# Kernel tuning notes

Hardware: AMD Instinct MI355X
Metric: run time of the kernel (lower is better)

The kernel has to match this reference:

```python
import jax, jax.numpy as jnp
import numpy as np
from jax import lax

L_MAX = 3          # n_ang_mom: l = 0, 1, 2
M_DIM = 2 * L_MAX - 1  # magnetic components, padded to 5
N_PAIRS = 40000
N_FEAT = 128


def hermite_features(g, n_features):
    """Orthonormal Hermite-function features h_0..h_{F-1}(g); [n] -> [n, F].

    Stable recurrence: h_{k+1} = sqrt(2/(k+1)) g h_k - sqrt(k/(k+1)) h_{k-1}.
    """
    h0 = (np.pi ** -0.25) * jnp.exp(-0.5 * g * g)
    h1 = jnp.sqrt(jnp.asarray(2.0, g.dtype)) * g * h0

    def step(carry, k):
        hkm1, hk = carry
        hkp1 = jnp.sqrt(2.0 / (k + 1.0)) * g * hk - jnp.sqrt(k / (k + 1.0)) * hkm1
        return (hk, hkp1), hkp1

    ks = jnp.arange(1, n_features - 1, dtype=g.dtype)  # produces h_2..h_{F-1}
    _, hs = lax.scan(step, (h0, h1), ks)
    feats = jnp.concatenate([h0[None], h1[None], hs], axis=0)  # [F, n]
    return feats.T  # [n, F]


def tensor_product(cg, a, b):
    """CG-style equivariant contraction.

    cg: [L, M, L, M, L, M] (sparse by selection rules), a, b: [L, M, n, F].
    out[l3, m3, n, f] = sum_{l1 m1 l2 m2} cg[l3,m3,l1,m1,l2,m2] a[l1,m1,n,f] b[l2,m2,n,f]
    """
    return jnp.einsum('lmabpq,abnf,pqnf->lmnf', cg, a, b)


def setup_inputs() -> dict:
    key = jax.random.key(0)
    k0, k1, k2, k3, k4 = jax.random.split(key, 5)
    L, M, N, F = L_MAX, M_DIM, N_PAIRS, N_FEAT
    x = jax.random.normal(k0, (L, M, N, F), dtype=jnp.float32)
    y = jax.random.normal(k1, (L, M, N, F), dtype=jnp.float32)
    g = jax.random.uniform(k2, (N,), dtype=jnp.float32, minval=0.5, maxval=5.0)
    scale = 1.0 / np.sqrt(F)  # GlorotNormal-like scaling
    w1 = jax.random.normal(k3, (F, F), dtype=jnp.float32) * scale
    w2 = jax.random.normal(k4, (F, F), dtype=jnp.float32) * scale
    # Clebsch-Gordan-like coefficient tensor with selection-rule sparsity:
    # nonzero only if |l1-l2| <= l3 <= l1+l2, |m_i| <= l_i, m3 == m1 + m2.
    rng = np.random.default_rng(0)
    cg = np.zeros((L, M, L, M, L, M), dtype=np.float32)
    c = L - 1  # m index offset: m -> m + c
    for l3 in range(L):
        for l1 in range(L):
            for l2 in range(L):
                if not (abs(l1 - l2) <= l3 <= l1 + l2):
                    continue
                for m1 in range(-l1, l1 + 1):
                    for m2 in range(-l2, l2 + 1):
                        m3 = m1 + m2
                        if abs(m3) <= l3:
                            cg[l3, m3 + c, l1, m1 + c, l2, m2 + c] = rng.standard_normal()
    return {"x": x, "y": y, "g": g, "w1": w1, "w2": w2, "cg": jnp.asarray(cg)}


def reference(x, y, g, w1, w2, cg):
    h = hermite_features(g, w1.shape[0])        # [n, F]
    w1g = jnp.einsum('fk,nk->nf', w1, h)        # [n, F]
    w2g = jnp.einsum('fk,nk->nf', w2, h)        # [n, F]
    a1 = w1g[None, None] * x                    # [L, M, n, F]
    b1 = w2g[None, None] * y
    a2 = w1g[None, None] * y
    b2 = w2g[None, None] * x
    res = tensor_product(cg, a1, b1) + tensor_product(cg, a2, b2)
    return res
```

## Files before the change

### kernel.cpp

```cpp
#include <hip/hip_runtime.h>
#include <array>

namespace {

constexpr int NPAIRS = 40000;
constexpr long NF = (long)NPAIRS * 128;

struct Term {
  int o, a, b;
};

constexpr int count_terms() {
  int idx = 0;
  for (int o = 0; o < 15; ++o) {
    const int l3 = o / 5, m3 = o % 5 - 2;
    if (m3 < -l3 || m3 > l3) continue;
    for (int l1 = 0; l1 < 3; ++l1)
      for (int l2 = 0; l2 < 3; ++l2) {
        const int ld = l1 > l2 ? l1 - l2 : l2 - l1;
        if (l3 < ld || l3 > l1 + l2) continue;
        const int mlo = (-l1 > m3 - l2) ? -l1 : m3 - l2;
        const int mhi = (l1 < m3 + l2) ? l1 : m3 + l2;
        for (int m1 = mlo; m1 <= mhi; ++m1) ++idx;
      }
  }
  return idx;
}
constexpr int NTERMS = count_terms();
static_assert(NTERMS == 117, "term count");

constexpr std::array<Term, NTERMS> make_terms() {
  std::array<Term, NTERMS> t{};
  int idx = 0;
  for (int o = 0; o < 15; ++o) {
    const int l3 = o / 5, m3 = o % 5 - 2;
    if (m3 < -l3 || m3 > l3) continue;
    for (int l1 = 0; l1 < 3; ++l1)
      for (int l2 = 0; l2 < 3; ++l2) {
        const int ld = l1 > l2 ? l1 - l2 : l2 - l1;
        if (l3 < ld || l3 > l1 + l2) continue;
        const int mlo = (-l1 > m3 - l2) ? -l1 : m3 - l2;
        const int mhi = (l1 < m3 + l2) ? l1 : m3 + l2;
        for (int m1 = mlo; m1 <= mhi; ++m1) {
          t[idx].o = o;
          t[idx].a = l1 * 5 + m1 + 2;
          t[idx].b = l2 * 5 + (m3 - m1) + 2;
          ++idx;
        }
      }
  }
  return t;
}
constexpr auto TERMS = make_terms();

constexpr std::array<int, 15> make_acc_idx() {
  std::array<int, 15> m{};
  for (int o = 0; o < 15; ++o) m[o] = -1;
  int q = 0;
  for (int o = 0; o < 15; ++o) {
    const int l3 = o / 5, m3 = o % 5 - 2;
    if (m3 >= -l3 && m3 <= l3) m[o] = q++;
  }
  return m;
}
constexpr auto ACC_IDX = make_acc_idx();

constexpr std::array<int, 9> make_used() {
  std::array<int, 9> u{};
  int q = 0;
  for (int o = 0; o < 15; ++o)
    if (ACC_IDX[o] >= 0) u[q++] = o;
  return u;
}
constexpr auto USED = make_used();

__global__ __launch_bounds__(256, 4) void s_kernel(const float* __restrict__ g,
                                                   const float* __restrict__ w1,
                                                   const float* __restrict__ w2,
                                                   float* __restrict__ s_out) {
  __shared__ float ht[128][32];
  __shared__ float wt1[16][132];
  __shared__ float wt2[16][132];

  const int tid = threadIdx.x;
  const int blk = blockIdx.x;

  if (tid < 32) {
    const float gv = g[blk * 32 + tid];
    float hkm1 = 0.75112554446494248286f * expf(-0.5f * gv * gv);
    float hk = 1.41421356237309504880f * gv * hkm1;
    ht[0][tid] = hkm1;
    ht[1][tid] = hk;
#pragma unroll 1
    for (int k = 1; k <= 126; ++k) {
      const float kf = (float)k;
      const float hkp1 =
          sqrtf(2.0f / (kf + 1.0f)) * gv * hk - sqrtf(kf / (kf + 1.0f)) * hkm1;
      ht[k + 1][tid] = hkp1;
      hkm1 = hk;
      hk = hkp1;
    }
  }

  const int fg = tid & 31;
  const int ng = tid >> 5;

  float acc1[4][4];
  float acc2[4][4];
#pragma unroll
  for (int i = 0; i < 4; ++i)
#pragma unroll
    for (int j = 0; j < 4; ++j) {
      acc1[i][j] = 0.f;
      acc2[i][j] = 0.f;
    }

  for (int kc = 0; kc < 8; ++kc) {
#pragma unroll
    for (int it = 0; it < 2; ++it) {
      const int lin = tid + it * 256;
      const int f = lin >> 2;
      const int kq = lin & 3;
      const float4 v1 = *(const float4*)(w1 + f * 128 + kc * 16 + kq * 4);
      const float4 v2 = *(const float4*)(w2 + f * 128 + kc * 16 + kq * 4);
      wt1[kq * 4 + 0][f] = v1.x;
      wt1[kq * 4 + 1][f] = v1.y;
      wt1[kq * 4 + 2][f] = v1.z;
      wt1[kq * 4 + 3][f] = v1.w;
      wt2[kq * 4 + 0][f] = v2.x;
      wt2[kq * 4 + 1][f] = v2.y;
      wt2[kq * 4 + 2][f] = v2.z;
      wt2[kq * 4 + 3][f] = v2.w;
    }
    __syncthreads();

#pragma unroll
    for (int kk = 0; kk < 16; ++kk) {
      const float4 wv1 = *(const float4*)&wt1[kk][fg * 4];
      const float4 wv2 = *(const float4*)&wt2[kk][fg * 4];
      const float4 ha = *(const float4*)&ht[kc * 16 + kk][ng * 4];
      const float hv[4] = {ha.x, ha.y, ha.z, ha.w};
#pragma unroll
      for (int i = 0; i < 4; ++i) {
        acc1[i][0] = fmaf(hv[i], wv1.x, acc1[i][0]);
        acc1[i][1] = fmaf(hv[i], wv1.y, acc1[i][1]);
        acc1[i][2] = fmaf(hv[i], wv1.z, acc1[i][2]);
        acc1[i][3] = fmaf(hv[i], wv1.w, acc1[i][3]);
        acc2[i][0] = fmaf(hv[i], wv2.x, acc2[i][0]);
        acc2[i][1] = fmaf(hv[i], wv2.y, acc2[i][1]);
        acc2[i][2] = fmaf(hv[i], wv2.z, acc2[i][2]);
        acc2[i][3] = fmaf(hv[i], wv2.w, acc2[i][3]);
      }
    }
    __syncthreads();
  }

#pragma unroll
  for (int i = 0; i < 4; ++i) {
    const long n = (long)blk * 32 + ng * 4 + i;
    float4 sv;
    sv.x = acc1[i][0] * acc2[i][0];
    sv.y = acc1[i][1] * acc2[i][1];
    sv.z = acc1[i][2] * acc2[i][2];
    sv.w = acc1[i][3] * acc2[i][3];
    *(float4*)(s_out + n * 128 + fg * 4) = sv;
  }
}

__global__ __attribute__((amdgpu_waves_per_eu(3, 4)))
__launch_bounds__(256) void tp_kernel(const float* __restrict__ x,
                                      const float* __restrict__ y,
                                      const float* __restrict__ cg,
                                      float* __restrict__ out) {
  __shared__ float d2s[NTERMS];
  const int tid = threadIdx.x;
  if (tid < NTERMS) {
    const Term tm = TERMS[tid];
    d2s[tid] = cg[(tm.o * 15 + tm.a) * 15 + tm.b] + cg[(tm.o * 15 + tm.b) * 15 + tm.a];
  }
  __syncthreads();

  const long off = (long)blockIdx.x * 1024 + tid * 4;

  float4 xv[9], yv[9];
#pragma unroll
  for (int q = 0; q < 9; ++q) xv[q] = *(const float4*)(x + (long)USED[q] * NF + off);
#pragma unroll
  for (int q = 0; q < 9; ++q) yv[q] = *(const float4*)(y + (long)USED[q] * NF + off);
  const float4 sv = *(const float4*)(out + off);
  __builtin_amdgcn_sched_barrier(0);

  float4 acc[9];
#pragma unroll
  for (int q = 0; q < 9; ++q) acc[q] = make_float4(0.f, 0.f, 0.f, 0.f);

#pragma unroll
  for (int t = 0; t < NTERMS; ++t) {
    const int qo = ACC_IDX[TERMS[t].o];
    const int qa = ACC_IDX[TERMS[t].a];
    const int qb = ACC_IDX[TERMS[t].b];
    const float c = d2s[t];
    acc[qo].x = fmaf(c, xv[qa].x * yv[qb].x, acc[qo].x);
    acc[qo].y = fmaf(c, xv[qa].y * yv[qb].y, acc[qo].y);
    acc[qo].z = fmaf(c, xv[qa].z * yv[qb].z, acc[qo].z);
    acc[qo].w = fmaf(c, xv[qa].w * yv[qb].w, acc[qo].w);
  }

#pragma unroll
  for (int o = 0; o < 15; ++o) {
    const int q = ACC_IDX[o];
    float4 r;
    if (q >= 0) {
      r.x = acc[q].x * sv.x;
      r.y = acc[q].y * sv.y;
      r.z = acc[q].z * sv.z;
      r.w = acc[q].w * sv.w;
    } else {
      r = make_float4(0.f, 0.f, 0.f, 0.f);
    }
    *(float4*)(out + (long)o * NF + off) = r;
  }
}

}

extern "C" void kernel_launch(void* const* d_in, const int* in_sizes, int n_in,
                              void* d_out, int out_size, void* d_ws, size_t ws_size,
                              hipStream_t stream) {
  const float* x = (const float*)d_in[0];
  const float* y = (const float*)d_in[1];
  const float* g = (const float*)d_in[2];
  const float* w1 = (const float*)d_in[3];
  const float* w2 = (const float*)d_in[4];
  const float* cg = (const float*)d_in[5];
  float* out = (float*)d_out;

  s_kernel<<<1250, 256, 0, stream>>>(g, w1, w2, out);
  tp_kernel<<<5000, 256, 0, stream>>>(x, y, cg, out);
}
```

Baseline: 238.1 us.

## Make tensor-product kernel persistent with double-buffered global-to-LDS DMA prefetch

The tensor-product kernel now runs as 250 persistent blocks, each walking 20 contiguous chunks. Inputs are streamed into a double-buffered shared-memory region with global_load_lds. The next chunk's x/y loads are issued while the current chunk is computed and stored, with a manual vmcnt wait controlling the pipeline. The aim is to keep memory requests in flight continuously instead of relying on many short-lived blocks. In exchange, the kernel uses about 147 KB of LDS, which limits it to one 4-wave block per CU, so latency hiding depends entirely on the explicit prefetch depth.

```diff
diff --git a/kernel.cpp b/kernel.cpp
--- a/kernel.cpp
+++ b/kernel.cpp
@@ -5,6 +5,11 @@
 
 constexpr int NPAIRS = 40000;
 constexpr long NF = (long)NPAIRS * 128;
+
+constexpr int CHUNK = 1024;
+constexpr int NCHUNKS = (int)(NF / CHUNK);
+constexpr int BLOCKS = 250;
+constexpr int CPB = NCHUNKS / BLOCKS;
 
 struct Term {
   int o, a, b;
@@ -74,6 +79,12 @@
 }
 constexpr auto USED = make_used();
 
+__device__ __forceinline__ void dma16(const float* gsrc, float* ldst) {
+  __builtin_amdgcn_global_load_lds(
+      (const __attribute__((address_space(1))) void*)gsrc,
+      (__attribute__((address_space(3))) void*)ldst, 16, 0, 0);
+}
+
 __global__ __launch_bounds__(256, 4) void s_kernel(const float* __restrict__ g,
                                                    const float* __restrict__ w1,
                                                    const float* __restrict__ w2,
@@ -167,12 +178,14 @@
   }
 }
 
-__global__ __attribute__((amdgpu_waves_per_eu(3, 4)))
+__global__ __attribute__((amdgpu_waves_per_eu(1, 2)))
 __launch_bounds__(256) void tp_kernel(const float* __restrict__ x,
                                       const float* __restrict__ y,
                                       const float* __restrict__ cg,
                                       float* __restrict__ out) {
-  __shared__ float d2s[NTERMS];
+  extern __shared__ float smem[];
+  float* d2s = smem + 2 * 18 * CHUNK;
+
   const int tid = threadIdx.x;
   if (tid < NTERMS) {
     const Term tm = TERMS[tid];
@@ -180,45 +193,77 @@
   }
   __syncthreads();
 
-  const long off = (long)blockIdx.x * 1024 + tid * 4;
-
-  float4 xv[9], yv[9];
-#pragma unroll
-  for (int q = 0; q < 9; ++q) xv[q] = *(const float4*)(x + (long)USED[q] * NF + off);
-#pragma unroll
-  for (int q = 0; q < 9; ++q) yv[q] = *(const float4*)(y + (long)USED[q] * NF + off);
-  const float4 sv = *(const float4*)(out + off);
-  __builtin_amdgcn_sched_barrier(0);
-
-  float4 acc[9];
-#pragma unroll
-  for (int q = 0; q < 9; ++q) acc[q] = make_float4(0.f, 0.f, 0.f, 0.f);
-
-#pragma unroll
-  for (int t = 0; t < NTERMS; ++t) {
-    const int qo = ACC_IDX[TERMS[t].o];
-    const int qa = ACC_IDX[TERMS[t].a];
-    const int qb = ACC_IDX[TERMS[t].b];
-    const float c = d2s[t];
-    acc[qo].x = fmaf(c, xv[qa].x * yv[qb].x, acc[qo].x);
-    acc[qo].y = fmaf(c, xv[qa].y * yv[qb].y, acc[qo].y);
-    acc[qo].z = fmaf(c, xv[qa].z * yv[qb].z, acc[qo].z);
-    acc[qo].w = fmaf(c, xv[qa].w * yv[qb].w, acc[qo].w);
-  }
-
-#pragma unroll
-  for (int o = 0; o < 15; ++o) {
-    const int q = ACC_IDX[o];
-    float4 r;
-    if (q >= 0) {
-      r.x = acc[q].x * sv.x;
-      r.y = acc[q].y * sv.y;
-      r.z = acc[q].z * sv.z;
-      r.w = acc[q].w * sv.w;
-    } else {
-      r = make_float4(0.f, 0.f, 0.f, 0.f);
-    }
-    *(float4*)(out + (long)o * NF + off) = r;
+  const int wv = tid >> 6;
+  const int lane = tid & 63;
+  const long base0 = (long)blockIdx.x * CPB * CHUNK;
+  const long lsrc = wv * 256 + lane * 4;
+
+  auto issue = [&](int i, int buf) {
+    const long goff = base0 + (long)i * CHUNK;
+    float* dst = smem + buf * (18 * CHUNK);
+#pragma unroll
+    for (int q = 0; q < 9; ++q)
+      dma16(x + (long)USED[q] * NF + goff + lsrc, dst + q * CHUNK + wv * 256);
+#pragma unroll
+    for (int q = 0; q < 9; ++q)
+      dma16(y + (long)USED[q] * NF + goff + lsrc, dst + (9 + q) * CHUNK + wv * 256);
+  };
+
+  issue(0, 0);
+  float4 svC = *(const float4*)(out + base0 + tid * 4);
+  asm volatile("" ::: "memory");
+  issue(1, 1);
+  float4 svN = *(const float4*)(out + base0 + CHUNK + tid * 4);
+
+  for (int i = 0; i < CPB; ++i) {
+    const int cur = i & 1;
+    asm volatile("s_waitcnt vmcnt(19)" ::: "memory");
+
+    const long goff = base0 + (long)i * CHUNK;
+    const float* L = smem + cur * (18 * CHUNK);
+
+    float4 xq[9], yq[9];
+#pragma unroll
+    for (int q = 0; q < 9; ++q) xq[q] = *(const float4*)(L + q * CHUNK + tid * 4);
+#pragma unroll
+    for (int q = 0; q < 9; ++q) yq[q] = *(const float4*)(L + (9 + q) * CHUNK + tid * 4);
+
+    float4 acc[9];
+#pragma unroll
+    for (int q = 0; q < 9; ++q) acc[q] = make_float4(0.f, 0.f, 0.f, 0.f);
+
+#pragma unroll
+    for (int t = 0; t < NTERMS; ++t) {
+      const int qo = ACC_IDX[TERMS[t].o];
+      const int qa = ACC_IDX[TERMS[t].a];
+      const int qb = ACC_IDX[TERMS[t].b];
+      const float c = d2s[t];
+      acc[qo].x = fmaf(c, xq[qa].x * yq[qb].x, acc[qo].x);
+      acc[qo].y = fmaf(c, xq[qa].y * yq[qb].y, acc[qo].y);
+      acc[qo].z = fmaf(c, xq[qa].z * yq[qb].z, acc[qo].z);
+      acc[qo].w = fmaf(c, xq[qa].w * yq[qb].w, acc[qo].w);
+    }
+
+#pragma unroll
+    for (int o = 0; o < 15; ++o) {
+      const int q = ACC_IDX[o];
+      float4 r;
+      if (q >= 0) {
+        r.x = acc[q].x * svC.x;
+        r.y = acc[q].y * svC.y;
+        r.z = acc[q].z * svC.z;
+        r.w = acc[q].w * svC.w;
+      } else {
+        r = make_float4(0.f, 0.f, 0.f, 0.f);
+      }
+      *(float4*)(out + (long)o * NF + goff + tid * 4) = r;
+    }
+
+    svC = svN;
+    if (i + 2 < CPB) {
+      issue(i + 2, cur);
+      svN = *(const float4*)(out + goff + 2 * CHUNK + tid * 4);
+    }
   }
 }
 
@@ -236,5 +281,6 @@
   float* out = (float*)d_out;
 
   s_kernel<<<1250, 256, 0, stream>>>(g, w1, w2, out);
-  tp_kernel<<<5000, 256, 0, stream>>>(x, y, cg, out);
-}
+  const size_t shmem = (size_t)(2 * 18 * CHUNK + 128) * sizeof(float);
+  tp_kernel<<<BLOCKS, 256, shmem, stream>>>(x, y, cg, out);
+}
```

After: 220.9 us. 1.08x faster.

## Move zero-plane stores into s_kernel and stage s in workspace

Applied to the files above, without the earlier changes.

The six always-zero output planes are now written by the compute-bound s_kernel instead of the bandwidth-bound tp_kernel, and the s product goes to workspace when it is large enough. tp_kernel then writes only the nine live planes. The sched_barrier is dropped and waves_per_eu is relaxed from 3 to 2. The aim is to hide the zero-fill traffic under s_kernel's GEMM-like compute and cut tp_kernel's store volume, at the cost of a slower s_kernel and a fallback path when the workspace is too small.

```diff
diff --git a/kernel.cpp b/kernel.cpp
--- a/kernel.cpp
+++ b/kernel.cpp
@@ -74,10 +74,14 @@
 }
 constexpr auto USED = make_used();
 
+__constant__ constexpr int ZPLANES[6] = {0, 1, 3, 4, 5, 9};
+
 __global__ __launch_bounds__(256, 4) void s_kernel(const float* __restrict__ g,
                                                    const float* __restrict__ w1,
                                                    const float* __restrict__ w2,
-                                                   float* __restrict__ s_out) {
+                                                   float* __restrict__ s_out,
+                                                   float* __restrict__ out,
+                                                   int zstart) {
   __shared__ float ht[128][32];
   __shared__ float wt1[16][132];
   __shared__ float wt2[16][132];
@@ -102,6 +106,17 @@
     }
   }
 
+  {
+    const long idx = (long)blk * 256 + tid;
+    const float4 z = make_float4(0.f, 0.f, 0.f, 0.f);
+    for (int zp = zstart; zp < 6; ++zp) {
+      float* base = out + (long)ZPLANES[zp] * NF;
+#pragma unroll
+      for (int r = 0; r < 4; ++r)
+        *(float4*)(base + (r * 320000 + idx) * 4) = z;
+    }
+  }
+
   const int fg = tid & 31;
   const int ng = tid >> 5;
 
@@ -167,11 +182,13 @@
   }
 }
 
-__global__ __attribute__((amdgpu_waves_per_eu(3, 4)))
+__global__ __attribute__((amdgpu_waves_per_eu(2, 4)))
 __launch_bounds__(256) void tp_kernel(const float* __restrict__ x,
                                       const float* __restrict__ y,
                                       const float* __restrict__ cg,
-                                      float* __restrict__ out) {
+                                      const float* __restrict__ s_in,
+                                      float* __restrict__ out,
+                                      int zero_p0) {
   __shared__ float d2s[NTERMS];
   const int tid = threadIdx.x;
   if (tid < NTERMS) {
@@ -187,8 +204,7 @@
   for (int q = 0; q < 9; ++q) xv[q] = *(const float4*)(x + (long)USED[q] * NF + off);
 #pragma unroll
   for (int q = 0; q < 9; ++q) yv[q] = *(const float4*)(y + (long)USED[q] * NF + off);
-  const float4 sv = *(const float4*)(out + off);
-  __builtin_amdgcn_sched_barrier(0);
+  const float4 sv = *(const float4*)(s_in + off);
 
   float4 acc[9];
 #pragma unroll
@@ -206,19 +222,18 @@
     acc[qo].w = fmaf(c, xv[qa].w * yv[qb].w, acc[qo].w);
   }
 
-#pragma unroll
-  for (int o = 0; o < 15; ++o) {
-    const int q = ACC_IDX[o];
+  if (zero_p0) {
+    *(float4*)(out + off) = make_float4(0.f, 0.f, 0.f, 0.f);
+  }
+
+#pragma unroll
+  for (int q = 0; q < 9; ++q) {
     float4 r;
-    if (q >= 0) {
-      r.x = acc[q].x * sv.x;
-      r.y = acc[q].y * sv.y;
-      r.z = acc[q].z * sv.z;
-      r.w = acc[q].w * sv.w;
-    } else {
-      r = make_float4(0.f, 0.f, 0.f, 0.f);
-    }
-    *(float4*)(out + (long)o * NF + off) = r;
+    r.x = acc[q].x * sv.x;
+    r.y = acc[q].y * sv.y;
+    r.z = acc[q].z * sv.z;
+    r.w = acc[q].w * sv.w;
+    *(float4*)(out + (long)USED[q] * NF + off) = r;
   }
 }
 
@@ -235,6 +250,10 @@
   const float* cg = (const float*)d_in[5];
   float* out = (float*)d_out;
 
-  s_kernel<<<1250, 256, 0, stream>>>(g, w1, w2, out);
-  tp_kernel<<<5000, 256, 0, stream>>>(x, y, cg, out);
-}
+  const size_t s_bytes = (size_t)NF * sizeof(float);
+  const bool use_ws = ws_size >= s_bytes;
+  float* s_buf = use_ws ? (float*)d_ws : out;
+
+  s_kernel<<<1250, 256, 0, stream>>>(g, w1, w2, s_buf, out, use_ws ? 0 : 1);
+  tp_kernel<<<5000, 256, 0, stream>>>(x, y, cg, s_buf, out, use_ws ? 0 : 1);
+}
```

Measured after the change: 216.0 us. 9.3% less time.

## Fuse Hermite-weight GEMM and tensor-product into one kernel with double-buffered loads

Applied to the files above, without the earlier changes.

Merges the s-computation kernel and the tensor-product kernel into a single launch. The per-pair scale no longer round-trips through global memory, and the second kernel launch goes away. Each thread now handles four pairs, with x/y loads double-buffered in registers to overlap memory with the CG contraction. The trade-off is much higher register pressure (four buffers of 9 float4 plus the GEMM accumulators), which lowers occupancy to about 2 waves/EU. The grid also shrinks to 1250 blocks, which may hurt latency hiding for this memory-bound workload.

```diff
diff --git a/kernel.cpp b/kernel.cpp
--- a/kernel.cpp
+++ b/kernel.cpp
@@ -74,16 +74,38 @@
 }
 constexpr auto USED = make_used();
 
-__global__ __launch_bounds__(256, 4) void s_kernel(const float* __restrict__ g,
-                                                   const float* __restrict__ w1,
-                                                   const float* __restrict__ w2,
-                                                   float* __restrict__ s_out) {
+__global__ __attribute__((amdgpu_waves_per_eu(2)))
+__launch_bounds__(256) void fused_kernel(const float* __restrict__ x,
+                                         const float* __restrict__ y,
+                                         const float* __restrict__ g,
+                                         const float* __restrict__ w1,
+                                         const float* __restrict__ w2,
+                                         const float* __restrict__ cg,
+                                         float* __restrict__ out) {
   __shared__ float ht[128][32];
   __shared__ float wt1[16][132];
   __shared__ float wt2[16][132];
+  __shared__ float d2s[NTERMS];
 
   const int tid = threadIdx.x;
   const int blk = blockIdx.x;
+
+  if (tid < NTERMS) {
+    const Term tm = TERMS[tid];
+    d2s[tid] = cg[(tm.o * 15 + tm.a) * 15 + tm.b] + cg[(tm.o * 15 + tm.b) * 15 + tm.a];
+  }
+
+  const int fg = tid & 31;
+  const int ng = tid >> 5;
+  const long n0 = (long)blk * 32 + ng * 4;
+  const long ebase = n0 * 128 + fg * 4;
+
+  float4 xvA[9], yvA[9], xvB[9], yvB[9];
+#pragma unroll
+  for (int q = 0; q < 9; ++q) xvA[q] = *(const float4*)(x + (long)USED[q] * NF + ebase);
+#pragma unroll
+  for (int q = 0; q < 9; ++q) yvA[q] = *(const float4*)(y + (long)USED[q] * NF + ebase);
+  __builtin_amdgcn_sched_barrier(0);
 
   if (tid < 32) {
     const float gv = g[blk * 32 + tid];
@@ -102,9 +124,6 @@
     }
   }
 
-  const int fg = tid & 31;
-  const int ng = tid >> 5;
-
   float acc1[4][4];
   float acc2[4][4];
 #pragma unroll
@@ -155,71 +174,65 @@
     __syncthreads();
   }
 
+  float4 sv[4];
 #pragma unroll
   for (int i = 0; i < 4; ++i) {
-    const long n = (long)blk * 32 + ng * 4 + i;
-    float4 sv;
-    sv.x = acc1[i][0] * acc2[i][0];
-    sv.y = acc1[i][1] * acc2[i][1];
-    sv.z = acc1[i][2] * acc2[i][2];
-    sv.w = acc1[i][3] * acc2[i][3];
-    *(float4*)(s_out + n * 128 + fg * 4) = sv;
-  }
-}
-
-__global__ __attribute__((amdgpu_waves_per_eu(3, 4)))
-__launch_bounds__(256) void tp_kernel(const float* __restrict__ x,
-                                      const float* __restrict__ y,
-                                      const float* __restrict__ cg,
-                                      float* __restrict__ out) {
-  __shared__ float d2s[NTERMS];
-  const int tid = threadIdx.x;
-  if (tid < NTERMS) {
-    const Term tm = TERMS[tid];
-    d2s[tid] = cg[(tm.o * 15 + tm.a) * 15 + tm.b] + cg[(tm.o * 15 + tm.b) * 15 + tm.a];
-  }
-  __syncthreads();
-
-  const long off = (long)blockIdx.x * 1024 + tid * 4;
-
-  float4 xv[9], yv[9];
-#pragma unroll
-  for (int q = 0; q < 9; ++q) xv[q] = *(const float4*)(x + (long)USED[q] * NF + off);
-#pragma unroll
-  for (int q = 0; q < 9; ++q) yv[q] = *(const float4*)(y + (long)USED[q] * NF + off);
-  const float4 sv = *(const float4*)(out + off);
-  __builtin_amdgcn_sched_barrier(0);
-
-  float4 acc[9];
-#pragma unroll
-  for (int q = 0; q < 9; ++q) acc[q] = make_float4(0.f, 0.f, 0.f, 0.f);
-
-#pragma unroll
-  for (int t = 0; t < NTERMS; ++t) {
-    const int qo = ACC_IDX[TERMS[t].o];
-    const int qa = ACC_IDX[TERMS[t].a];
-    const int qb = ACC_IDX[TERMS[t].b];
-    const float c = d2s[t];
-    acc[qo].x = fmaf(c, xv[qa].x * yv[qb].x, acc[qo].x);
-    acc[qo].y = fmaf(c, xv[qa].y * yv[qb].y, acc[qo].y);
-    acc[qo].z = fmaf(c, xv[qa].z * yv[qb].z, acc[qo].z);
-    acc[qo].w = fmaf(c, xv[qa].w * yv[qb].w, acc[qo].w);
-  }
-
-#pragma unroll
-  for (int o = 0; o < 15; ++o) {
-    const int q = ACC_IDX[o];
-    float4 r;
-    if (q >= 0) {
-      r.x = acc[q].x * sv.x;
-      r.y = acc[q].y * sv.y;
-      r.z = acc[q].z * sv.z;
-      r.w = acc[q].w * sv.w;
-    } else {
-      r = make_float4(0.f, 0.f, 0.f, 0.f);
-    }
-    *(float4*)(out + (long)o * NF + off) = r;
-  }
+    sv[i].x = acc1[i][0] * acc2[i][0];
+    sv[i].y = acc1[i][1] * acc2[i][1];
+    sv[i].z = acc1[i][2] * acc2[i][2];
+    sv[i].w = acc1[i][3] * acc2[i][3];
+  }
+
+  auto issue = [&](float4* xb, float4* yb, long eoff) {
+#pragma unroll
+    for (int q = 0; q < 9; ++q) xb[q] = *(const float4*)(x + (long)USED[q] * NF + eoff);
+#pragma unroll
+    for (int q = 0; q < 9; ++q) yb[q] = *(const float4*)(y + (long)USED[q] * NF + eoff);
+  };
+  auto compute_store = [&](const float4* xb, const float4* yb, float4 s, long eoff) {
+    float4 acc[9];
+#pragma unroll
+    for (int q = 0; q < 9; ++q) acc[q] = make_float4(0.f, 0.f, 0.f, 0.f);
+#pragma unroll
+    for (int t = 0; t < NTERMS; ++t) {
+      const int qo = ACC_IDX[TERMS[t].o];
+      const int qa = ACC_IDX[TERMS[t].a];
+      const int qb = ACC_IDX[TERMS[t].b];
+      const float c = d2s[t];
+      acc[qo].x = fmaf(c, xb[qa].x * yb[qb].x, acc[qo].x);
+      acc[qo].y = fmaf(c, xb[qa].y * yb[qb].y, acc[qo].y);
+      acc[qo].z = fmaf(c, xb[qa].z * yb[qb].z, acc[qo].z);
+      acc[qo].w = fmaf(c, xb[qa].w * yb[qb].w, acc[qo].w);
+    }
+#pragma unroll
+    for (int o = 0; o < 15; ++o) {
+      const int q = ACC_IDX[o];
+      float4 r;
+      if (q >= 0) {
+        r.x = acc[q].x * s.x;
+        r.y = acc[q].y * s.y;
+        r.z = acc[q].z * s.z;
+        r.w = acc[q].w * s.w;
+      } else {
+        r = make_float4(0.f, 0.f, 0.f, 0.f);
+      }
+      *(float4*)(out + (long)o * NF + eoff) = r;
+    }
+  };
+
+  issue(xvB, yvB, ebase + 128);
+  __builtin_amdgcn_sched_barrier(0);
+  compute_store(xvA, yvA, sv[0], ebase);
+
+  issue(xvA, yvA, ebase + 256);
+  __builtin_amdgcn_sched_barrier(0);
+  compute_store(xvB, yvB, sv[1], ebase + 128);
+
+  issue(xvB, yvB, ebase + 384);
+  __builtin_amdgcn_sched_barrier(0);
+  compute_store(xvA, yvA, sv[2], ebase + 256);
+
+  compute_store(xvB, yvB, sv[3], ebase + 384);
 }
 
 }
@@ -235,6 +248,5 @@
   const float* cg = (const float*)d_in[5];
   float* out = (float*)d_out;
 
-  s_kernel<<<1250, 256, 0, stream>>>(g, w1, w2, out);
-  tp_kernel<<<5000, 256, 0, stream>>>(x, y, cg, out);
-}
+  fused_kernel<<<1250, 256, 0, stream>>>(x, y, g, w1, w2, cg, out);
+}
```

New measurement: 637.1 us. +167.6%, slower.
